# Performance work log

Measured on AMD Instinct MI355X. Metric: run time of the kernel, lower is better.

The kernel has to match this reference:

```python
import jax, jax.numpy as jnp
import numpy as np

S, B, I, H = 2048, 64, 128, 128
E = float(np.e)


def setup_inputs() -> dict:
    key = jax.random.key(0)
    ks = jax.random.split(key, 16)
    s = 1.0 / np.sqrt(H)
    inp = {
        "x": jax.random.normal(ks[0], (S, B, I), jnp.float32),
        "h0": jnp.zeros((2, B, H), jnp.float32),
        "c0": jnp.zeros((2, B, H), jnp.float32),
        # elapsed times, strictly positive
        "delta_ts": jax.random.uniform(ks[1], (B, S), jnp.float32, 0.1, 10.0),
    }
    names = ["W_ih", "W_hh", "b_ih", "b_hh", "W_d", "b_d"]
    shapes = [(4 * H, I), (4 * H, H), (4 * H,), (4 * H,), (H, H), (H,)]
    idx = 2
    for d in ["f", "r"]:
        for n, sh in zip(names, shapes):
            inp[f"{n}_{d}"] = jax.random.uniform(ks[idx], sh, jnp.float32, -s, s)
            idx += 1
    return inp


def _run_dir(x, dt, h, c, W_ih, W_hh, b_ih, b_hh, W_d, b_d):
    """Scan a TLSTM cell over time. x: [S,B,I], dt: [S,B]."""
    def step(carry, inp):
        h, c = carry
        xt, dtt = inp
        # time-aware memory decomposition (Baytas et al.)
        c_s = jnp.tanh(c @ W_d.T + b_d)               # short-term memory
        c_adj = c - c_s + c_s / jnp.log(E + dtt[:, None])  # discounted by elapsed time
        gates = xt @ W_ih.T + b_ih + h @ W_hh.T + b_hh
        i_g, f_g, g_g, o_g = jnp.split(gates, 4, axis=-1)
        c_n = jax.nn.sigmoid(f_g) * c_adj + jax.nn.sigmoid(i_g) * jnp.tanh(g_g)
        h_n = jax.nn.sigmoid(o_g) * jnp.tanh(c_n)
        return (h_n, c_n), h_n

    (h, c), ys = jax.lax.scan(step, (h, c), (x, dt))
    return ys, h, c


def reference(x, h0, c0, delta_ts,
              W_ih_f, W_hh_f, b_ih_f, b_hh_f, W_d_f, b_d_f,
              W_ih_r, W_hh_r, b_ih_r, b_hh_r, W_d_r, b_d_r):
    dt = delta_ts.T  # [S, B]
    out_f, _, _ = _run_dir(x, dt, h0[0], c0[0],
                           W_ih_f, W_hh_f, b_ih_f, b_hh_f, W_d_f, b_d_f)
    out_r, _, _ = _run_dir(x[::-1], dt[::-1], h0[1], c0[1],
                           W_ih_r, W_hh_r, b_ih_r, b_hh_r, W_d_r, b_d_r)
    return jnp.concatenate([out_f, out_r[::-1]], axis=-1)  # [S, B, 2H]
```

## Files before the change

### kernel.cpp

```cpp
#include <hip/hip_runtime.h>
#include <hip/hip_bf16.h>

#define SEQ  2048
#define BAT  64
#define HID  128
#define LDSP 136

#define XB_OFF  (1u << 20)
#define IL_OFF  (35u << 20)

typedef __bf16 bf16x8 __attribute__((ext_vector_type(8)));
typedef float  f32x4  __attribute__((ext_vector_type(4)));

#define MFMA(a,b,c) __builtin_amdgcn_mfma_f32_16x16x32_bf16((a),(b),(c),0,0,0)

__device__ __forceinline__ float sig_f(float x) {
    return __fdividef(1.0f, 1.0f + __expf(-x));
}
__device__ __forceinline__ float tanh_f(float x) {
    return 1.0f - __fdividef(2.0f, 1.0f + __expf(2.0f * x));
}
__device__ __forceinline__ bf16x8 cvt8(const float* p) {
    bf16x8 r;
    #pragma unroll
    for (int i = 0; i < 8; ++i) r[i] = (__bf16)p[i];
    return r;
}

__global__ void cvt_x_kernel(const float* __restrict__ x, __bf16* __restrict__ xb) {
    const int i = (blockIdx.x * 256 + threadIdx.x) * 4;
    const float4 v = *reinterpret_cast<const float4*>(x + i);
    __bf16 o[4];
    o[0] = (__bf16)v.x; o[1] = (__bf16)v.y; o[2] = (__bf16)v.z; o[3] = (__bf16)v.w;
    *reinterpret_cast<uint2*>(xb + i) = *reinterpret_cast<const uint2*>(o);
}

__global__ void prep_ilog_kernel(const float* __restrict__ dts, float* __restrict__ il) {
    const int idx = blockIdx.x * 256 + threadIdx.x;
    const int b = idx >> 11, t = idx & 2047;
    const float l = __logf(2.718281828459045f + dts[idx]);
    il[t * BAT + b] = __fdividef(1.0f, l) - 1.0f;
}

__global__ __launch_bounds__(512, 2) void tlstm_main(
    const __bf16* __restrict__ xb,   const float* __restrict__ ilg,
    const float* __restrict__ h0,    const float* __restrict__ c0,
    const float* __restrict__ Wih_f, const float* __restrict__ Whh_f,
    const float* __restrict__ bih_f, const float* __restrict__ bhh_f,
    const float* __restrict__ Wd_f,  const float* __restrict__ bd_f,
    const float* __restrict__ Wih_r, const float* __restrict__ Whh_r,
    const float* __restrict__ bih_r, const float* __restrict__ bhh_r,
    const float* __restrict__ Wd_r,  const float* __restrict__ bd_r,
    float* __restrict__ out)
{
    const int d    = blockIdx.x >> 4;
    const int b0   = (blockIdx.x & 15) * 4;
    const int tid  = threadIdx.x;
    const int w    = tid >> 6;
    const int lane = tid & 63;
    const int nl   = lane & 15;
    const int q    = lane >> 4;
    const int j    = w * 16 + nl;

    const float* Wih = d ? Wih_r : Wih_f;
    const float* Whh = d ? Whh_r : Whh_f;
    const float* bih = d ? bih_r : bih_f;
    const float* bhh = d ? bhh_r : bhh_f;
    const float* Wd  = d ? Wd_r  : Wd_f;
    const float* bd  = d ? bd_r  : bd_f;

    __shared__ __align__(16) __bf16 hc_a[2][16][LDSP];

    bf16x8 whh_fr[4][4], wih_fr[4][4], wd_fr[4];
    #pragma unroll
    for (int g = 0; g < 4; ++g) {
        const int row = g * 128 + j;
        #pragma unroll
        for (int kt = 0; kt < 4; ++kt) {
            const int off = row * HID + kt * 32 + q * 8;
            wih_fr[g][kt] = cvt8(Wih + off);
            whh_fr[g][kt] = cvt8(Whh + off);
        }
    }
    #pragma unroll
    for (int kt = 0; kt < 4; ++kt)
        wd_fr[kt] = cvt8(Wd + j * HID + kt * 32 + q * 8);

    float bias_g[4];
    #pragma unroll
    for (int g = 0; g < 4; ++g)
        bias_g[g] = bih[g * 128 + j] + bhh[g * 128 + j];
    const float bias_d = bd[j];

    for (int e = tid; e < 4 * HID; e += 512) {
        const int ci = e >> 7, k = e & 127;
        hc_a[0][ci * 4][k]     = (__bf16)h0[(d * BAT + b0 + ci) * HID + k];
        hc_a[0][ci * 4 + 1][k] = (__bf16)c0[(d * BAT + b0 + ci) * HID + k];
    }
    float c_st = c0[(d * BAT + b0 + q) * HID + j];
    __syncthreads();

    const int t0      = d ? (SEQ - 1) : 0;
    const int tstep   = d ? -1 : 1;
    const int xstride = tstep * BAT * HID;
    const int istride = tstep * BAT;
    const int ostride = tstep * BAT * 256;

    const __bf16* xp = xb + (size_t)(t0 * BAT + b0 + (nl >> 2)) * HID + q * 8;
    const float*  ip = ilg + (size_t)t0 * BAT + b0 + q;
    float*        op = out + (size_t)(t0 * BAT + b0 + q) * 256 + d * 128 + j;

    bf16x8 xfrA[4], xfrB[4];
    float  ilA, ilB;
    f32x4  xaccA[4], xaccB[4];

    #pragma unroll
    for (int kt = 0; kt < 4; ++kt)
        xfrA[kt] = *reinterpret_cast<const bf16x8*>(xp + kt * 32);
    ilA = *ip;
    #pragma unroll
    for (int g = 0; g < 4; ++g)
        xaccA[g] = f32x4{bias_g[g], bias_g[g], bias_g[g], bias_g[g]};
    #pragma unroll
    for (int kt = 0; kt < 4; ++kt) {
        xaccA[0] = MFMA(xfrA[kt], wih_fr[0][kt], xaccA[0]);
        xaccA[1] = MFMA(xfrA[kt], wih_fr[1][kt], xaccA[1]);
        xaccA[2] = MFMA(xfrA[kt], wih_fr[2][kt], xaccA[2]);
        xaccA[3] = MFMA(xfrA[kt], wih_fr[3][kt], xaccA[3]);
    }
    xp += xstride; ip += istride;
    #pragma unroll
    for (int kt = 0; kt < 4; ++kt)
        xfrB[kt] = *reinterpret_cast<const bf16x8*>(xp + kt * 32);
    ilB = *ip;

    auto lstm_step = [&](int p, f32x4 (&accIn)[4], f32x4 (&accOut)[4],
                         bf16x8 (&xfrIn)[4], bf16x8 (&xfrLd)[4],
                         float& ilBuf) __attribute__((always_inline)) {
        f32x4 ai = accIn[0], af = accIn[1], ag = accIn[2], ao = accIn[3];
        f32x4 acs = f32x4{bias_d, bias_d, bias_d, bias_d};

        bf16x8 hcfr[4];
        #pragma unroll
        for (int kt = 0; kt < 4; ++kt)
            hcfr[kt] = *reinterpret_cast<const bf16x8*>(&hc_a[p][nl][kt * 32 + q * 8]);

        #pragma unroll
        for (int kt = 0; kt < 4; ++kt) {
            ai  = MFMA(hcfr[kt], whh_fr[0][kt], ai);
            af  = MFMA(hcfr[kt], whh_fr[1][kt], af);
            ag  = MFMA(hcfr[kt], whh_fr[2][kt], ag);
            ao  = MFMA(hcfr[kt], whh_fr[3][kt], ao);
            acs = MFMA(hcfr[kt], wd_fr[kt], acs);
        }

        xp += xstride; ip += istride;
        #pragma unroll
        for (int kt = 0; kt < 4; ++kt)
            xfrLd[kt] = *reinterpret_cast<const bf16x8*>(xp + kt * 32);
        const float il2 = *ip;

        const int pn = p ^ 1;
        {
            const float cs   = tanh_f(acs[1]);
            const float cadj = fmaf(cs, ilBuf, c_st);
            const float gi   = sig_f(ai[0]);
            const float gf   = sig_f(af[0]);
            const float gg   = tanh_f(ag[0]);
            const float go   = sig_f(ao[0]);
            const float cn   = gf * cadj + gi * gg;
            const float hn   = go * tanh_f(cn);
            c_st = cn;
            hc_a[pn][q * 4][j]     = (__bf16)hn;
            hc_a[pn][q * 4 + 1][j] = (__bf16)cn;
            *op = hn;
        }
        op += ostride;
        ilBuf = il2;

        #pragma unroll
        for (int g = 0; g < 4; ++g)
            accOut[g] = f32x4{bias_g[g], bias_g[g], bias_g[g], bias_g[g]};
        #pragma unroll
        for (int kt = 0; kt < 4; ++kt) {
            accOut[0] = MFMA(xfrIn[kt], wih_fr[0][kt], accOut[0]);
            accOut[1] = MFMA(xfrIn[kt], wih_fr[1][kt], accOut[1]);
            accOut[2] = MFMA(xfrIn[kt], wih_fr[2][kt], accOut[2]);
            accOut[3] = MFMA(xfrIn[kt], wih_fr[3][kt], accOut[3]);
        }

        asm volatile("s_waitcnt lgkmcnt(0)\n\ts_barrier" ::: "memory");
    };

    for (int ts = 0; ts < SEQ; ts += 2) {
        lstm_step(0, xaccA, xaccB, xfrB, xfrA, ilA);
        lstm_step(1, xaccB, xaccA, xfrA, xfrB, ilB);
    }
}

extern "C" void kernel_launch(void* const* d_in, const int* in_sizes, int n_in,
                              void* d_out, int out_size, void* d_ws, size_t ws_size,
                              hipStream_t stream) {
    const float* x     = (const float*)d_in[0];
    const float* h0    = (const float*)d_in[1];
    const float* c0    = (const float*)d_in[2];
    const float* dts   = (const float*)d_in[3];
    const float* Wih_f = (const float*)d_in[4];
    const float* Whh_f = (const float*)d_in[5];
    const float* bih_f = (const float*)d_in[6];
    const float* bhh_f = (const float*)d_in[7];
    const float* Wd_f  = (const float*)d_in[8];
    const float* bd_f  = (const float*)d_in[9];
    const float* Wih_r = (const float*)d_in[10];
    const float* Whh_r = (const float*)d_in[11];
    const float* bih_r = (const float*)d_in[12];
    const float* bhh_r = (const float*)d_in[13];
    const float* Wd_r  = (const float*)d_in[14];
    const float* bd_r  = (const float*)d_in[15];
    float* out = (float*)d_out;

    __bf16* xbuf = (__bf16*)((char*)d_ws + XB_OFF);
    float*  il   = (float*)((char*)d_ws + IL_OFF);

    cvt_x_kernel<<<16384, 256, 0, stream>>>(x, xbuf);
    prep_ilog_kernel<<<512, 256, 0, stream>>>(dts, il);

    tlstm_main<<<32, 512, 0, stream>>>(xbuf, il, h0, c0,
                                       Wih_f, Whh_f, bih_f, bhh_f, Wd_f, bd_f,
                                       Wih_r, Whh_r, bih_r, bhh_r, Wd_r, bd_r,
                                       out);
}
```

Measured before the change: 2.013 ms.

## Batch input projection across 4-timestep windows using idle MFMA rows

In the old code the x·W_ih MFMA filled 16 rows with only 4 distinct batch rows, wasting three quarters of each instruction. Now the 16 rows pack 4 batches times 4 timesteps, so one window's input projection is computed in 4 MFMAs per gate instead of 16 over four steps. Each step broadcasts its precomputed scalar into the recurrent accumulators and loads x and the log factors one window ahead. This cuts MFMA work off the serial recurrence path but adds register pressure and more complex indexing.

Measured after the change: 2.279 ms. 13.2% more time.

```diff
diff --git a/kernel.cpp b/kernel.cpp
--- a/kernel.cpp
+++ b/kernel.cpp
@@ -106,95 +106,115 @@
     const int istride = tstep * BAT;
     const int ostride = tstep * BAT * 256;
 
-    const __bf16* xp = xb + (size_t)(t0 * BAT + b0 + (nl >> 2)) * HID + q * 8;
-    const float*  ip = ilg + (size_t)t0 * BAT + b0 + q;
-    float*        op = out + (size_t)(t0 * BAT + b0 + q) * 256 + d * 128 + j;
+    const __bf16* xp0 = xb + (size_t)((t0 + tstep * (nl & 3)) * BAT + b0 + (nl >> 2)) * HID + q * 8;
+    const float*  ip0 = ilg + (size_t)t0 * BAT + b0 + q;
+    float*        op  = out + (size_t)(t0 * BAT + b0 + q) * 256 + d * 128 + j;
 
     bf16x8 xfrA[4], xfrB[4];
-    float  ilA, ilB;
     f32x4  xaccA[4], xaccB[4];
-
+    float  ilA[4], ilB[4];
+
+    {
+        bf16x8 x0[4];
+        #pragma unroll
+        for (int kt = 0; kt < 4; ++kt)
+            x0[kt] = *reinterpret_cast<const bf16x8*>(xp0 + kt * 32);
+        #pragma unroll
+        for (int g = 0; g < 4; ++g)
+            xaccA[g] = f32x4{bias_g[g], bias_g[g], bias_g[g], bias_g[g]};
+        #pragma unroll
+        for (int kt = 0; kt < 4; ++kt) {
+            xaccA[0] = MFMA(x0[kt], wih_fr[0][kt], xaccA[0]);
+            xaccA[1] = MFMA(x0[kt], wih_fr[1][kt], xaccA[1]);
+            xaccA[2] = MFMA(x0[kt], wih_fr[2][kt], xaccA[2]);
+            xaccA[3] = MFMA(x0[kt], wih_fr[3][kt], xaccA[3]);
+        }
+    }
     #pragma unroll
     for (int kt = 0; kt < 4; ++kt)
-        xfrA[kt] = *reinterpret_cast<const bf16x8*>(xp + kt * 32);
-    ilA = *ip;
-    #pragma unroll
-    for (int g = 0; g < 4; ++g)
-        xaccA[g] = f32x4{bias_g[g], bias_g[g], bias_g[g], bias_g[g]};
-    #pragma unroll
-    for (int kt = 0; kt < 4; ++kt) {
-        xaccA[0] = MFMA(xfrA[kt], wih_fr[0][kt], xaccA[0]);
-        xaccA[1] = MFMA(xfrA[kt], wih_fr[1][kt], xaccA[1]);
-        xaccA[2] = MFMA(xfrA[kt], wih_fr[2][kt], xaccA[2]);
-        xaccA[3] = MFMA(xfrA[kt], wih_fr[3][kt], xaccA[3]);
-    }
-    xp += xstride; ip += istride;
-    #pragma unroll
-    for (int kt = 0; kt < 4; ++kt)
-        xfrB[kt] = *reinterpret_cast<const bf16x8*>(xp + kt * 32);
-    ilB = *ip;
-
-    auto lstm_step = [&](int p, f32x4 (&accIn)[4], f32x4 (&accOut)[4],
-                         bf16x8 (&xfrIn)[4], bf16x8 (&xfrLd)[4],
-                         float& ilBuf) __attribute__((always_inline)) {
-        f32x4 ai = accIn[0], af = accIn[1], ag = accIn[2], ao = accIn[3];
-        f32x4 acs = f32x4{bias_d, bias_d, bias_d, bias_d};
-
-        bf16x8 hcfr[4];
-        #pragma unroll
-        for (int kt = 0; kt < 4; ++kt)
-            hcfr[kt] = *reinterpret_cast<const bf16x8*>(&hc_a[p][nl][kt * 32 + q * 8]);
-
-        #pragma unroll
-        for (int kt = 0; kt < 4; ++kt) {
-            ai  = MFMA(hcfr[kt], whh_fr[0][kt], ai);
-            af  = MFMA(hcfr[kt], whh_fr[1][kt], af);
-            ag  = MFMA(hcfr[kt], whh_fr[2][kt], ag);
-            ao  = MFMA(hcfr[kt], whh_fr[3][kt], ao);
-            acs = MFMA(hcfr[kt], wd_fr[kt], acs);
+        xfrA[kt] = *reinterpret_cast<const bf16x8*>(xp0 + 4 * xstride + kt * 32);
+    #pragma unroll
+    for (int dt = 0; dt < 4; ++dt)
+        ilA[dt] = ip0[dt * istride];
+
+    const __bf16* xpl = xp0 + 8 * xstride;
+    const float*  ipl = ip0 + 4 * istride;
+
+    auto window = [&](f32x4 (&xaccCur)[4], f32x4 (&xaccNext)[4],
+                      bf16x8 (&xfrUse)[4], bf16x8 (&xfrLd)[4],
+                      float (&ilCur)[4], float (&ilNext)[4]) __attribute__((always_inline)) {
+        #pragma unroll
+        for (int dt = 0; dt < 4; ++dt) {
+            const int p = dt & 1;
+
+            bf16x8 hcfr[4];
+            #pragma unroll
+            for (int kt = 0; kt < 4; ++kt)
+                hcfr[kt] = *reinterpret_cast<const bf16x8*>(&hc_a[p][nl][kt * 32 + q * 8]);
+
+            {
+                const bf16x8 xf = xfrUse[dt];
+                if (dt == 0) {
+                    #pragma unroll
+                    for (int g = 0; g < 4; ++g) {
+                        const f32x4 binit = f32x4{bias_g[g], bias_g[g], bias_g[g], bias_g[g]};
+                        xaccNext[g] = MFMA(xf, wih_fr[g][0], binit);
+                    }
+                } else {
+                    #pragma unroll
+                    for (int g = 0; g < 4; ++g)
+                        xaccNext[g] = MFMA(xf, wih_fr[g][dt], xaccNext[g]);
+                }
+            }
+
+            f32x4 ai, af, ag, ao;
+            {
+                const float s0 = xaccCur[0][dt], s1 = xaccCur[1][dt];
+                const float s2 = xaccCur[2][dt], s3 = xaccCur[3][dt];
+                ai = f32x4{s0, s0, s0, s0};
+                af = f32x4{s1, s1, s1, s1};
+                ag = f32x4{s2, s2, s2, s2};
+                ao = f32x4{s3, s3, s3, s3};
+            }
+            f32x4 acs = f32x4{bias_d, bias_d, bias_d, bias_d};
+            #pragma unroll
+            for (int kt = 0; kt < 4; ++kt) {
+                ai  = MFMA(hcfr[kt], whh_fr[0][kt], ai);
+                af  = MFMA(hcfr[kt], whh_fr[1][kt], af);
+                ag  = MFMA(hcfr[kt], whh_fr[2][kt], ag);
+                ao  = MFMA(hcfr[kt], whh_fr[3][kt], ao);
+                acs = MFMA(hcfr[kt], wd_fr[kt], acs);
+            }
+
+            xfrLd[dt]  = *reinterpret_cast<const bf16x8*>(xpl + dt * 32);
+            ilNext[dt] = ipl[dt * istride];
+
+            const int pn = p ^ 1;
+            {
+                const float cs   = tanh_f(acs[1]);
+                const float cadj = fmaf(cs, ilCur[dt], c_st);
+                const float gi   = sig_f(ai[0]);
+                const float gf   = sig_f(af[0]);
+                const float gg   = tanh_f(ag[0]);
+                const float go   = sig_f(ao[0]);
+                const float cn   = gf * cadj + gi * gg;
+                const float hn   = go * tanh_f(cn);
+                c_st = cn;
+                hc_a[pn][q * 4][j]     = (__bf16)hn;
+                hc_a[pn][q * 4 + 1][j] = (__bf16)cn;
+                *op = hn;
+            }
+            op += ostride;
+
+            asm volatile("s_waitcnt lgkmcnt(0)\n\ts_barrier" ::: "memory");
         }
-
-        xp += xstride; ip += istride;
-        #pragma unroll
-        for (int kt = 0; kt < 4; ++kt)
-            xfrLd[kt] = *reinterpret_cast<const bf16x8*>(xp + kt * 32);
-        const float il2 = *ip;
-
-        const int pn = p ^ 1;
-        {
-            const float cs   = tanh_f(acs[1]);
-            const float cadj = fmaf(cs, ilBuf, c_st);
-            const float gi   = sig_f(ai[0]);
-            const float gf   = sig_f(af[0]);
-            const float gg   = tanh_f(ag[0]);
-            const float go   = sig_f(ao[0]);
-            const float cn   = gf * cadj + gi * gg;
-            const float hn   = go * tanh_f(cn);
-            c_st = cn;
-            hc_a[pn][q * 4][j]     = (__bf16)hn;
-            hc_a[pn][q * 4 + 1][j] = (__bf16)cn;
-            *op = hn;
-        }
-        op += ostride;
-        ilBuf = il2;
-
-        #pragma unroll
-        for (int g = 0; g < 4; ++g)
-            accOut[g] = f32x4{bias_g[g], bias_g[g], bias_g[g], bias_g[g]};
-        #pragma unroll
-        for (int kt = 0; kt < 4; ++kt) {
-            accOut[0] = MFMA(xfrIn[kt], wih_fr[0][kt], accOut[0]);
-            accOut[1] = MFMA(xfrIn[kt], wih_fr[1][kt], accOut[1]);
-            accOut[2] = MFMA(xfrIn[kt], wih_fr[2][kt], accOut[2]);
-            accOut[3] = MFMA(xfrIn[kt], wih_fr[3][kt], accOut[3]);
-        }
-
-        asm volatile("s_waitcnt lgkmcnt(0)\n\ts_barrier" ::: "memory");
+        xpl += 4 * xstride;
+        ipl += 4 * istride;
     };
 
-    for (int ts = 0; ts < SEQ; ts += 2) {
-        lstm_step(0, xaccA, xaccB, xfrB, xfrA, ilA);
-        lstm_step(1, xaccB, xaccA, xfrA, xfrB, ilB);
+    for (int wn = 0; wn < SEQ / 4; wn += 2) {
+        window(xaccA, xaccB, xfrA, xfrB, ilA, ilB);
+        window(xaccB, xaccA, xfrB, xfrA, ilB, ilA);
     }
 }
 
```
